# Kernel optimization log

Measured on AMD Instinct MI355X. Metric: run time of the kernel, lower is better.

The kernel has to match this reference:

```python
import jax, jax.numpy as jnp
import numpy as np

N, E, F_IN, H, C = 50000, 800000, 128, 4, 32
HC = H * C
NEG_SLOPE = 0.2


def setup_inputs() -> dict:
    key = jax.random.key(0)
    ks = jax.random.split(key, 20)
    def w(k, shape, fan_in):
        return jax.random.normal(k, shape, jnp.float32) * (1.0 / np.sqrt(fan_in))
    inp = {
        'x': jax.random.normal(ks[0], (N, F_IN), jnp.float32),
        'edge_index': jax.random.randint(ks[1], (2, E), 0, N, jnp.int64),
        # layer 1: in F_IN -> H*C
        'Wl1': w(ks[2], (F_IN, HC), F_IN), 'Wr1': w(ks[3], (F_IN, HC), F_IN),
        'att1': w(ks[4], (H, C), C), 'b1': jnp.zeros((HC,), jnp.float32),
        # layer 2: in H*C -> H*C
        'Wl2': w(ks[5], (HC, HC), HC), 'Wr2': w(ks[6], (HC, HC), HC),
        'att2': w(ks[7], (H, C), C), 'b2': jnp.zeros((HC,), jnp.float32),
        # layer 3
        'Wl3': w(ks[8], (HC, HC), HC), 'Wr3': w(ks[9], (HC, HC), HC),
        'att3': w(ks[10], (H, C), C), 'b3': jnp.zeros((HC,), jnp.float32),
        # final fc: H*C -> 1
        'Wf': w(ks[11], (HC, 1), HC), 'bf': jnp.zeros((1,), jnp.float32),
    }
    return inp


def gatv2_layer(x, src, dst, Wl, Wr, att, b):
    n = x.shape[0]
    xl = (x @ Wl).reshape(n, H, C)  # source transform
    xr = (x @ Wr).reshape(n, H, C)  # target transform
    z = xl[src] + xr[dst]                                  # [E', H, C]
    e = jnp.sum(jax.nn.leaky_relu(z, NEG_SLOPE) * att, axis=-1)  # [E', H]
    m = jax.ops.segment_max(e, dst, num_segments=n)        # segment softmax
    a = jnp.exp(e - m[dst])
    denom = jax.ops.segment_sum(a, dst, num_segments=n)
    alpha = a / denom[dst]                                 # [E', H]
    out = jax.ops.segment_sum(alpha[:, :, None] * xl[src], dst, num_segments=n)
    return out.reshape(n, HC) + b


def reference(x, edge_index, Wl1, Wr1, att1, b1, Wl2, Wr2, att2, b2, Wl3, Wr3, att3, b3, Wf, bf):
    n = x.shape[0]
    loops = jnp.arange(n, dtype=edge_index.dtype)
    src = jnp.concatenate([edge_index[0], loops])  # PyG adds self loops
    dst = jnp.concatenate([edge_index[1], loops])
    h = jax.nn.relu(gatv2_layer(x, src, dst, Wl1, Wr1, att1, b1))
    h = jax.nn.relu(gatv2_layer(h, src, dst, Wl2, Wr2, att2, b2))
    h = jax.nn.relu(gatv2_layer(h, src, dst, Wl3, Wr3, att3, b3))
    return (h @ Wf + bf)[:, 0]  # [N]
```

## Files before the change

### kernel.cpp

```cpp
#include <hip/hip_runtime.h>
#include <hip/hip_fp16.h>

constexpr int FDIM = 128;
constexpr float SLOPE = 0.2f;

using half8 = __attribute__((ext_vector_type(8))) _Float16;
using f32x4 = __attribute__((ext_vector_type(4))) float;

__device__ __forceinline__ float lrelu(float x) {
  return x > 0.f ? x : x * SLOPE;
}

struct F8 { float4 a, b; };
__device__ __forceinline__ F8 cvt8(uint4 u) {
  union { uint4 u; __half2 h[4]; } t;
  t.u = u;
  float2 f0 = __half22float2(t.h[0]);
  float2 f1 = __half22float2(t.h[1]);
  float2 f2 = __half22float2(t.h[2]);
  float2 f3 = __half22float2(t.h[3]);
  F8 r;
  r.a = make_float4(f0.x, f0.y, f1.x, f1.y);
  r.b = make_float4(f2.x, f2.y, f3.x, f3.y);
  return r;
}

__global__ __launch_bounds__(256) void prep_w(
    const float* __restrict__ W0, const float* __restrict__ W1,
    const float* __restrict__ W2, const float* __restrict__ W3,
    const float* __restrict__ W4, const float* __restrict__ W5,
    __half* __restrict__ Wt) {
  const float* Ws[6] = {W0, W1, W2, W3, W4, W5};
  const float* W = Ws[blockIdx.x];
  __half* o = Wt + (size_t)blockIdx.x * FDIM * FDIM;
  const int t = threadIdx.x;
  const int c4 = (t & 31) * 4;
#pragma unroll
  for (int rep = 0; rep < 16; ++rep) {
    int k = (t >> 5) + rep * 8;
    float4 v = *(const float4*)(W + (size_t)k * FDIM + c4);
    o[(size_t)(c4 + 0) * FDIM + k] = __float2half(v.x);
    o[(size_t)(c4 + 1) * FDIM + k] = __float2half(v.y);
    o[(size_t)(c4 + 2) * FDIM + k] = __float2half(v.z);
    o[(size_t)(c4 + 3) * FDIM + k] = __float2half(v.w);
  }
}

__global__ __launch_bounds__(512, 4) void gemm_mfma(
    const float* __restrict__ hin, const __half* __restrict__ Wlt,
    const __half* __restrict__ Wrt, __half* __restrict__ xl,
    __half* __restrict__ xr, int n) {
  __shared__ __half Ah[128][40];
  __shared__ __half Bsl[2][128][40];
  const int tid = threadIdx.x;
  const int row0 = blockIdx.x * 128;
  const int wv = tid >> 6;
  const int lane = tid & 63;
  const int sel = wv >> 2;
  const int rb = wv & 3;
  const int l15 = lane & 15;
  const int l4 = lane >> 4;

  f32x4 acc[2][8];
#pragma unroll
  for (int i = 0; i < 2; ++i)
#pragma unroll
    for (int j = 0; j < 8; ++j) acc[i][j] = (f32x4){0.f, 0.f, 0.f, 0.f};

  const int sr = tid >> 2;
  const int sc = (tid & 3) * 8;
  const int bslab = tid >> 8;
  const int bidx = tid & 255;
  const int bc = bidx >> 1;
  const int bko = (bidx & 1) * 16;
  const __half* Wsrc = bslab ? Wrt : Wlt;
  const int gr = row0 + sr;

  for (int k0 = 0; k0 < 128; k0 += 32) {
    if (k0) __syncthreads();
    {
      float4 v0 = make_float4(0.f, 0.f, 0.f, 0.f), v1 = v0;
      if (gr < n) {
        v0 = *(const float4*)(hin + (size_t)gr * FDIM + k0 + sc);
        v1 = *(const float4*)(hin + (size_t)gr * FDIM + k0 + sc + 4);
      }
      __half* dst = &Ah[sr][sc];
      dst[0] = __float2half(v0.x); dst[1] = __float2half(v0.y);
      dst[2] = __float2half(v0.z); dst[3] = __float2half(v0.w);
      dst[4] = __float2half(v1.x); dst[5] = __float2half(v1.y);
      dst[6] = __float2half(v1.z); dst[7] = __float2half(v1.w);
    }
    {
      const uint4* src = (const uint4*)(Wsrc + (size_t)bc * FDIM + k0 + bko);
      uint4 w0 = src[0], w1 = src[1];
      *(uint4*)&Bsl[bslab][bc][bko] = w0;
      *(uint4*)&Bsl[bslab][bc][bko + 8] = w1;
    }
    __syncthreads();
    half8 a0 = *(const half8*)&Ah[rb * 32 + l15][l4 * 8];
    half8 a1 = *(const half8*)&Ah[rb * 32 + 16 + l15][l4 * 8];
#pragma unroll
    for (int nf = 0; nf < 8; ++nf) {
      half8 b = *(const half8*)&Bsl[sel][nf * 16 + l15][l4 * 8];
      acc[0][nf] = __builtin_amdgcn_mfma_f32_16x16x32_f16(a0, b, acc[0][nf], 0, 0, 0);
      acc[1][nf] = __builtin_amdgcn_mfma_f32_16x16x32_f16(a1, b, acc[1][nf], 0, 0, 0);
    }
  }

  __half* out = sel ? xr : xl;
#pragma unroll
  for (int af = 0; af < 2; ++af) {
#pragma unroll
    for (int nf = 0; nf < 8; ++nf) {
      int col = nf * 16 + l15;
#pragma unroll
      for (int r = 0; r < 4; ++r) {
        int row = row0 + rb * 32 + af * 16 + l4 * 4 + r;
        if (row < n) out[(size_t)row * FDIM + col] = __float2half(acc[af][nf][r]);
      }
    }
  }
}

__global__ __launch_bounds__(256) void hist_dst(const int* __restrict__ dstI,
                                                int* __restrict__ deg, int e_cnt) {
  int i = blockIdx.x * blockDim.x + threadIdx.x;
  int stride = gridDim.x * blockDim.x;
  for (; i < e_cnt; i += stride) atomicAdd(&deg[dstI[i]], 1);
}

__global__ __launch_bounds__(1024) void scan_local(
    const int* __restrict__ deg, int* __restrict__ rowptr,
    int* __restrict__ btot, int n) {
  __shared__ int lds[1024];
  const int t = threadIdx.x;
  const int i = blockIdx.x * 1024 + t;
  int v = (i < n) ? deg[i] : 0;
  lds[t] = v;
  __syncthreads();
  for (int off = 1; off < 1024; off <<= 1) {
    int u = (t >= off) ? lds[t - off] : 0;
    __syncthreads();
    lds[t] += u;
    __syncthreads();
  }
  if (i < n) rowptr[i] = lds[t] - v;
  if (t == 1023) btot[blockIdx.x] = lds[1023];
}

__global__ __launch_bounds__(1024) void scan_btot(int* __restrict__ btot, int nb) {
  __shared__ int lds[1024];
  const int t = threadIdx.x;
  int v = (t < nb) ? btot[t] : 0;
  lds[t] = v;
  __syncthreads();
  for (int off = 1; off < 1024; off <<= 1) {
    int u = (t >= off) ? lds[t - off] : 0;
    __syncthreads();
    lds[t] += u;
    __syncthreads();
  }
  if (t < nb) btot[t] = lds[t] - v;
}

__global__ __launch_bounds__(1024) void scan_add(
    int* __restrict__ rowptr, int* __restrict__ rowcur,
    const int* __restrict__ btot, int n, int e_cnt) {
  const int i = blockIdx.x * 1024 + threadIdx.x;
  if (i < n) {
    int v = rowptr[i] + btot[blockIdx.x];
    rowptr[i] = v;
    rowcur[i] = v;
  }
  if (i == 0) rowptr[n] = e_cnt;
}

__global__ __launch_bounds__(256) void scatter_csr(
    const int* __restrict__ srcI, const int* __restrict__ dstI,
    int* __restrict__ rowcur, int* __restrict__ csr, int e_cnt) {
  int i = blockIdx.x * blockDim.x + threadIdx.x;
  int stride = gridDim.x * blockDim.x;
  for (; i < e_cnt; i += stride) {
    int pos = atomicAdd(&rowcur[dstI[i]], 1);
    csr[pos] = srcI[i];
  }
}

template <int LAST>
__global__ __launch_bounds__(256) void fused_attn(
    const __half* __restrict__ xl, const __half* __restrict__ xr,
    const int* __restrict__ rowptr, const int* __restrict__ csr,
    const float* __restrict__ att, const float* __restrict__ bias,
    const float* __restrict__ Wf, const float* __restrict__ bf,
    float* __restrict__ out, int n) {
  const int nid = (int)((blockIdx.x * (size_t)blockDim.x + threadIdx.x) >> 6);
  const int lane = threadIdx.x & 63;
  if (nid >= n) return;
  const int g = lane >> 4;
  const int q = lane & 15;
  const int f8 = q * 8;
  const float4 attA = *(const float4*)(att + f8);
  const float4 attB = *(const float4*)(att + f8 + 4);
  const F8 xrv = cvt8(*(const uint4*)(xr + (size_t)nid * FDIM + f8));
  const F8 xld = cvt8(*(const uint4*)(xl + (size_t)nid * FDIM + f8));
  const float4 xrA = xrv.a, xrB = xrv.b;
  const float4 xldA = xld.a, xldB = xld.b;

  float ps = fmaf(lrelu(xldA.x + xrA.x), attA.x,
             fmaf(lrelu(xldA.y + xrA.y), attA.y,
             fmaf(lrelu(xldA.z + xrA.z), attA.z,
             fmaf(lrelu(xldA.w + xrA.w), attA.w,
             fmaf(lrelu(xldB.x + xrB.x), attB.x,
             fmaf(lrelu(xldB.y + xrB.y), attB.y,
             fmaf(lrelu(xldB.z + xrB.z), attB.z,
                  lrelu(xldB.w + xrB.w) * attB.w)))))));
  ps += __shfl_xor(ps, 1);
  ps += __shfl_xor(ps, 2);

  float m = (g == 0) ? ps : -1e30f;
  float s = (g == 0) ? 1.f : 0.f;
  float4 accA = (g == 0) ? xldA : make_float4(0.f, 0.f, 0.f, 0.f);
  float4 accB = (g == 0) ? xldB : make_float4(0.f, 0.f, 0.f, 0.f);

  const int rs = rowptr[nid], re = rowptr[nid + 1];
  int jj = rs + g;
  bool v = jj < re;
  int sidx = v ? csr[jj] : 0;
  uint4 cur = make_uint4(0u, 0u, 0u, 0u);
  if (v) cur = *(const uint4*)(xl + (size_t)sidx * FDIM + f8);

  for (int t = rs; t < re; t += 4) {
    int jn = t + 4 + g;
    bool vn = jn < re;
    int sn = vn ? csr[jn] : 0;
    uint4 nxt = make_uint4(0u, 0u, 0u, 0u);
    if (vn) nxt = *(const uint4*)(xl + (size_t)sn * FDIM + f8);
    F8 xa = cvt8(cur);
    float4 xaA = xa.a, xaB = xa.b;
    float p = fmaf(lrelu(xaA.x + xrA.x), attA.x,
              fmaf(lrelu(xaA.y + xrA.y), attA.y,
              fmaf(lrelu(xaA.z + xrA.z), attA.z,
              fmaf(lrelu(xaA.w + xrA.w), attA.w,
              fmaf(lrelu(xaB.x + xrB.x), attB.x,
              fmaf(lrelu(xaB.y + xrB.y), attB.y,
              fmaf(lrelu(xaB.z + xrB.z), attB.z,
                   lrelu(xaB.w + xrB.w) * attB.w)))))));
    p += __shfl_xor(p, 1);
    p += __shfl_xor(p, 2);
    if (v) {
      float mn = fmaxf(m, p);
      float sc = __expf(m - mn);
      float w = __expf(p - mn);
      s = fmaf(s, sc, w);
      accA.x = fmaf(accA.x, sc, w * xaA.x);
      accA.y = fmaf(accA.y, sc, w * xaA.y);
      accA.z = fmaf(accA.z, sc, w * xaA.z);
      accA.w = fmaf(accA.w, sc, w * xaA.w);
      accB.x = fmaf(accB.x, sc, w * xaB.x);
      accB.y = fmaf(accB.y, sc, w * xaB.y);
      accB.z = fmaf(accB.z, sc, w * xaB.z);
      accB.w = fmaf(accB.w, sc, w * xaB.w);
      m = mn;
    }
    v = vn; cur = nxt;
  }

#pragma unroll
  for (int off = 16; off <= 32; off <<= 1) {
    float mo = __shfl_xor(m, off);
    float so = __shfl_xor(s, off);
    float4 aoA, aoB;
    aoA.x = __shfl_xor(accA.x, off); aoA.y = __shfl_xor(accA.y, off);
    aoA.z = __shfl_xor(accA.z, off); aoA.w = __shfl_xor(accA.w, off);
    aoB.x = __shfl_xor(accB.x, off); aoB.y = __shfl_xor(accB.y, off);
    aoB.z = __shfl_xor(accB.z, off); aoB.w = __shfl_xor(accB.w, off);
    float M = fmaxf(m, mo);
    float e0 = __expf(m - M), e1 = __expf(mo - M);
    s = fmaf(s, e0, so * e1);
    accA.x = fmaf(accA.x, e0, aoA.x * e1);
    accA.y = fmaf(accA.y, e0, aoA.y * e1);
    accA.z = fmaf(accA.z, e0, aoA.z * e1);
    accA.w = fmaf(accA.w, e0, aoA.w * e1);
    accB.x = fmaf(accB.x, e0, aoB.x * e1);
    accB.y = fmaf(accB.y, e0, aoB.y * e1);
    accB.z = fmaf(accB.z, e0, aoB.z * e1);
    accB.w = fmaf(accB.w, e0, aoB.w * e1);
    m = M;
  }

  const float inv = 1.f / s;
  const float4 bA = *(const float4*)(bias + f8);
  const float4 bB = *(const float4*)(bias + f8 + 4);
  float o0 = fmaxf(fmaf(accA.x, inv, bA.x), 0.f);
  float o1 = fmaxf(fmaf(accA.y, inv, bA.y), 0.f);
  float o2 = fmaxf(fmaf(accA.z, inv, bA.z), 0.f);
  float o3 = fmaxf(fmaf(accA.w, inv, bA.w), 0.f);
  float o4 = fmaxf(fmaf(accB.x, inv, bB.x), 0.f);
  float o5 = fmaxf(fmaf(accB.y, inv, bB.y), 0.f);
  float o6 = fmaxf(fmaf(accB.z, inv, bB.z), 0.f);
  float o7 = fmaxf(fmaf(accB.w, inv, bB.w), 0.f);

  if (LAST == 0) {
    if (g == 0) {
      *(float4*)(out + (size_t)nid * FDIM + f8) = make_float4(o0, o1, o2, o3);
      *(float4*)(out + (size_t)nid * FDIM + f8 + 4) = make_float4(o4, o5, o6, o7);
    }
  } else {
    const float4 wA = *(const float4*)(Wf + f8);
    const float4 wB = *(const float4*)(Wf + f8 + 4);
    float y = fmaf(o0, wA.x, fmaf(o1, wA.y, fmaf(o2, wA.z,
              fmaf(o3, wA.w, fmaf(o4, wB.x, fmaf(o5, wB.y,
              fmaf(o6, wB.z, o7 * wB.w)))))));
    y += __shfl_xor(y, 1);
    y += __shfl_xor(y, 2);
    y += __shfl_xor(y, 4);
    y += __shfl_xor(y, 8);
    if (lane == 0) out[nid] = y + bf[0];
  }
}

extern "C" void kernel_launch(void* const* d_in, const int* in_sizes, int n_in,
                              void* d_out, int out_size, void* d_ws, size_t ws_size,
                              hipStream_t stream) {
  const float* x = (const float*)d_in[0];
  const int* ei = (const int*)d_in[1];
  const int n = in_sizes[0] / FDIM;
  const int e_cnt = in_sizes[1] / 2;
  const int* srcI = ei;
  const int* dstI = ei + e_cnt;

  const float* Wl[3]  = {(const float*)d_in[2], (const float*)d_in[6], (const float*)d_in[10]};
  const float* Wr[3]  = {(const float*)d_in[3], (const float*)d_in[7], (const float*)d_in[11]};
  const float* att[3] = {(const float*)d_in[4], (const float*)d_in[8], (const float*)d_in[12]};
  const float* bs[3]  = {(const float*)d_in[5], (const float*)d_in[9], (const float*)d_in[13]};
  const float* Wf = (const float*)d_in[14];
  const float* bf = (const float*)d_in[15];

  __half* xlh = (__half*)d_ws;
  __half* xrh = xlh + (size_t)n * FDIM;
  float* hbuf = (float*)(xrh + (size_t)n * FDIM);
  int* deg    = (int*)(hbuf + (size_t)n * FDIM);
  int* rowptr = deg + n;
  int* rowcur = rowptr + n + 1;
  int* csr    = rowcur + n;
  int* btot   = csr + e_cnt;
  __half* Wt  = (__half*)(btot + 1024);

  const int nb = (n + 1023) / 1024;

  prep_w<<<6, 256, 0, stream>>>(Wl[0], Wr[0], Wl[1], Wr[1], Wl[2], Wr[2], Wt);
  hipMemsetAsync(deg, 0, (size_t)n * sizeof(int), stream);
  hist_dst<<<(e_cnt + 255) / 256, 256, 0, stream>>>(dstI, deg, e_cnt);
  scan_local<<<nb, 1024, 0, stream>>>(deg, rowptr, btot, n);
  scan_btot<<<1, 1024, 0, stream>>>(btot, nb);
  scan_add<<<nb, 1024, 0, stream>>>(rowptr, rowcur, btot, n, e_cnt);
  scatter_csr<<<(e_cnt + 255) / 256, 256, 0, stream>>>(srcI, dstI, rowcur, csr, e_cnt);

  const float* hin = x;
  const int gemmGrid = (n + 127) / 128;
  const int nodeBlocks = (n + 3) / 4;

  for (int L = 0; L < 3; ++L) {
    const __half* Wlt = Wt + (size_t)(2 * L) * FDIM * FDIM;
    const __half* Wrt = Wt + (size_t)(2 * L + 1) * FDIM * FDIM;
    gemm_mfma<<<gemmGrid, 512, 0, stream>>>(hin, Wlt, Wrt, xlh, xrh, n);
    if (L < 2) {
      fused_attn<0><<<nodeBlocks, 256, 0, stream>>>(xlh, xrh, rowptr, csr, att[L],
                                                    bs[L], nullptr, nullptr, hbuf, n);
      hin = hbuf;
    } else {
      fused_attn<1><<<nodeBlocks, 256, 0, stream>>>(xlh, xrh, rowptr, csr, att[L],
                                                    bs[L], Wf, bf, (float*)d_out, n);
    }
  }
}
```

Baseline: 384.9 us.

## Use fp16 intermediate activations, packed fp16 dot2 logits, and deeper gather prefetch

Layer outputs are now stored as fp16 rather than fp32, so the next GEMM loads half-width rows directly without converting them. The edge logit is computed with packed half2 add, leaky-relu and fdot2 instead of eight scalar fp32 FMAs, and attention weights are rounded to fp16. The neighbour gather now prefetches two edges ahead instead of one. Together these cut memory traffic and ALU work in the attention and GEMM kernels, at the cost of lower precision in the logits and activations and higher register pressure.

```diff
diff --git a/kernel.cpp b/kernel.cpp
--- a/kernel.cpp
+++ b/kernel.cpp
@@ -6,23 +6,28 @@
 
 using half8 = __attribute__((ext_vector_type(8))) _Float16;
 using f32x4 = __attribute__((ext_vector_type(4))) float;
-
-__device__ __forceinline__ float lrelu(float x) {
-  return x > 0.f ? x : x * SLOPE;
-}
-
-struct F8 { float4 a, b; };
-__device__ __forceinline__ F8 cvt8(uint4 u) {
-  union { uint4 u; __half2 h[4]; } t;
-  t.u = u;
-  float2 f0 = __half22float2(t.h[0]);
-  float2 f1 = __half22float2(t.h[1]);
-  float2 f2 = __half22float2(t.h[2]);
-  float2 f3 = __half22float2(t.h[3]);
-  F8 r;
-  r.a = make_float4(f0.x, f0.y, f1.x, f1.y);
-  r.b = make_float4(f2.x, f2.y, f3.x, f3.y);
-  return r;
+using h2v   = __attribute__((ext_vector_type(2))) _Float16;
+
+union H2U { __half2 s; h2v v; unsigned int u; };
+
+__device__ __forceinline__ float fdot2f(h2v a, h2v b, float c) {
+  return __builtin_amdgcn_fdot2(a, b, c, false);
+}
+
+union U4 { uint4 u; __half2 h[4]; };
+
+__device__ __forceinline__ float edge_logit(const __half2* xa2, const __half2* xr2,
+                                            const h2v* att2, h2v c02) {
+  float p = 0.f;
+#pragma unroll
+  for (int j = 0; j < 4; ++j) {
+    H2U ua, ur;
+    ua.s = xa2[j]; ur.s = xr2[j];
+    h2v z = ua.v + ur.v;
+    h2v lr = __builtin_elementwise_max(z, z * c02);
+    p = fdot2f(lr, att2[j], p);
+  }
+  return p;
 }
 
 __global__ __launch_bounds__(256) void prep_w(
@@ -46,8 +51,9 @@
   }
 }
 
+template <typename TIN>
 __global__ __launch_bounds__(512, 4) void gemm_mfma(
-    const float* __restrict__ hin, const __half* __restrict__ Wlt,
+    const TIN* __restrict__ hin, const __half* __restrict__ Wlt,
     const __half* __restrict__ Wrt, __half* __restrict__ xl,
     __half* __restrict__ xr, int n) {
   __shared__ __half Ah[128][40];
@@ -79,16 +85,23 @@
   for (int k0 = 0; k0 < 128; k0 += 32) {
     if (k0) __syncthreads();
     {
-      float4 v0 = make_float4(0.f, 0.f, 0.f, 0.f), v1 = v0;
-      if (gr < n) {
-        v0 = *(const float4*)(hin + (size_t)gr * FDIM + k0 + sc);
-        v1 = *(const float4*)(hin + (size_t)gr * FDIM + k0 + sc + 4);
+      union { uint4 u; __half h[8]; } pk;
+      if constexpr (sizeof(TIN) == 4) {
+        float4 v0 = make_float4(0.f, 0.f, 0.f, 0.f), v1 = v0;
+        if (gr < n) {
+          v0 = *(const float4*)((const float*)hin + (size_t)gr * FDIM + k0 + sc);
+          v1 = *(const float4*)((const float*)hin + (size_t)gr * FDIM + k0 + sc + 4);
+        }
+        pk.h[0] = __float2half(v0.x); pk.h[1] = __float2half(v0.y);
+        pk.h[2] = __float2half(v0.z); pk.h[3] = __float2half(v0.w);
+        pk.h[4] = __float2half(v1.x); pk.h[5] = __float2half(v1.y);
+        pk.h[6] = __float2half(v1.z); pk.h[7] = __float2half(v1.w);
+      } else {
+        pk.u = make_uint4(0u, 0u, 0u, 0u);
+        if (gr < n)
+          pk.u = *(const uint4*)((const __half*)hin + (size_t)gr * FDIM + k0 + sc);
       }
-      __half* dst = &Ah[sr][sc];
-      dst[0] = __float2half(v0.x); dst[1] = __float2half(v0.y);
-      dst[2] = __float2half(v0.z); dst[3] = __float2half(v0.w);
-      dst[4] = __float2half(v1.x); dst[5] = __float2half(v1.y);
-      dst[6] = __float2half(v1.z); dst[7] = __float2half(v1.w);
+      *(uint4*)&Ah[sr][sc] = pk.u;
     }
     {
       const uint4* src = (const uint4*)(Wsrc + (size_t)bc * FDIM + k0 + bko);
@@ -192,130 +205,111 @@
     const int* __restrict__ rowptr, const int* __restrict__ csr,
     const float* __restrict__ att, const float* __restrict__ bias,
     const float* __restrict__ Wf, const float* __restrict__ bf,
-    float* __restrict__ out, int n) {
+    void* __restrict__ outp, int n) {
   const int nid = (int)((blockIdx.x * (size_t)blockDim.x + threadIdx.x) >> 6);
   const int lane = threadIdx.x & 63;
   if (nid >= n) return;
   const int g = lane >> 4;
   const int q = lane & 15;
   const int f8 = q * 8;
-  const float4 attA = *(const float4*)(att + f8);
-  const float4 attB = *(const float4*)(att + f8 + 4);
-  const F8 xrv = cvt8(*(const uint4*)(xr + (size_t)nid * FDIM + f8));
-  const F8 xld = cvt8(*(const uint4*)(xl + (size_t)nid * FDIM + f8));
-  const float4 xrA = xrv.a, xrB = xrv.b;
-  const float4 xldA = xld.a, xldB = xld.b;
-
-  float ps = fmaf(lrelu(xldA.x + xrA.x), attA.x,
-             fmaf(lrelu(xldA.y + xrA.y), attA.y,
-             fmaf(lrelu(xldA.z + xrA.z), attA.z,
-             fmaf(lrelu(xldA.w + xrA.w), attA.w,
-             fmaf(lrelu(xldB.x + xrB.x), attB.x,
-             fmaf(lrelu(xldB.y + xrB.y), attB.y,
-             fmaf(lrelu(xldB.z + xrB.z), attB.z,
-                  lrelu(xldB.w + xrB.w) * attB.w)))))));
+  const h2v c02 = {(_Float16)SLOPE, (_Float16)SLOPE};
+  const float4 aA = *(const float4*)(att + f8);
+  const float4 aB = *(const float4*)(att + f8 + 4);
+  h2v att2[4] = {{(_Float16)aA.x, (_Float16)aA.y}, {(_Float16)aA.z, (_Float16)aA.w},
+                 {(_Float16)aB.x, (_Float16)aB.y}, {(_Float16)aB.z, (_Float16)aB.w}};
+  U4 xru, xlu;
+  xru.u = *(const uint4*)(xr + (size_t)nid * FDIM + f8);
+  xlu.u = *(const uint4*)(xl + (size_t)nid * FDIM + f8);
+
+  float ps = edge_logit(xlu.h, xru.h, att2, c02);
   ps += __shfl_xor(ps, 1);
   ps += __shfl_xor(ps, 2);
 
   float m = (g == 0) ? ps : -1e30f;
   float s = (g == 0) ? 1.f : 0.f;
-  float4 accA = (g == 0) ? xldA : make_float4(0.f, 0.f, 0.f, 0.f);
-  float4 accB = (g == 0) ? xldB : make_float4(0.f, 0.f, 0.f, 0.f);
+  float acc[8];
+#pragma unroll
+  for (int j = 0; j < 4; ++j) {
+    float2 f = __half22float2(xlu.h[j]);
+    acc[2 * j] = (g == 0) ? f.x : 0.f;
+    acc[2 * j + 1] = (g == 0) ? f.y : 0.f;
+  }
 
   const int rs = rowptr[nid], re = rowptr[nid + 1];
-  int jj = rs + g;
-  bool v = jj < re;
-  int sidx = v ? csr[jj] : 0;
-  uint4 cur = make_uint4(0u, 0u, 0u, 0u);
-  if (v) cur = *(const uint4*)(xl + (size_t)sidx * FDIM + f8);
+  const int j0 = rs + g;
+  bool v0 = j0 < re, v1 = (j0 + 4) < re;
+  U4 cur, nx1;
+  cur.u = make_uint4(0u, 0u, 0u, 0u);
+  nx1.u = cur.u;
+  if (v0) cur.u = *(const uint4*)(xl + (size_t)csr[j0] * FDIM + f8);
+  if (v1) nx1.u = *(const uint4*)(xl + (size_t)csr[j0 + 4] * FDIM + f8);
 
   for (int t = rs; t < re; t += 4) {
-    int jn = t + 4 + g;
-    bool vn = jn < re;
-    int sn = vn ? csr[jn] : 0;
-    uint4 nxt = make_uint4(0u, 0u, 0u, 0u);
-    if (vn) nxt = *(const uint4*)(xl + (size_t)sn * FDIM + f8);
-    F8 xa = cvt8(cur);
-    float4 xaA = xa.a, xaB = xa.b;
-    float p = fmaf(lrelu(xaA.x + xrA.x), attA.x,
-              fmaf(lrelu(xaA.y + xrA.y), attA.y,
-              fmaf(lrelu(xaA.z + xrA.z), attA.z,
-              fmaf(lrelu(xaA.w + xrA.w), attA.w,
-              fmaf(lrelu(xaB.x + xrB.x), attB.x,
-              fmaf(lrelu(xaB.y + xrB.y), attB.y,
-              fmaf(lrelu(xaB.z + xrB.z), attB.z,
-                   lrelu(xaB.w + xrB.w) * attB.w)))))));
+    const int jn = t + 8 + g;
+    const bool vn = jn < re;
+    U4 nx2;
+    nx2.u = make_uint4(0u, 0u, 0u, 0u);
+    if (vn) nx2.u = *(const uint4*)(xl + (size_t)csr[jn] * FDIM + f8);
+
+    float p = edge_logit(cur.h, xru.h, att2, c02);
     p += __shfl_xor(p, 1);
     p += __shfl_xor(p, 2);
-    if (v) {
+    if (v0) {
       float mn = fmaxf(m, p);
       float sc = __expf(m - mn);
       float w = __expf(p - mn);
       s = fmaf(s, sc, w);
-      accA.x = fmaf(accA.x, sc, w * xaA.x);
-      accA.y = fmaf(accA.y, sc, w * xaA.y);
-      accA.z = fmaf(accA.z, sc, w * xaA.z);
-      accA.w = fmaf(accA.w, sc, w * xaA.w);
-      accB.x = fmaf(accB.x, sc, w * xaB.x);
-      accB.y = fmaf(accB.y, sc, w * xaB.y);
-      accB.z = fmaf(accB.z, sc, w * xaB.z);
-      accB.w = fmaf(accB.w, sc, w * xaB.w);
+#pragma unroll
+      for (int j = 0; j < 4; ++j) {
+        acc[2 * j] = fmaf(acc[2 * j], sc, w * (float)__low2half(cur.h[j]));
+        acc[2 * j + 1] = fmaf(acc[2 * j + 1], sc, w * (float)__high2half(cur.h[j]));
+      }
       m = mn;
     }
-    v = vn; cur = nxt;
+    v0 = v1; v1 = vn; cur = nx1; nx1 = nx2;
   }
 
 #pragma unroll
   for (int off = 16; off <= 32; off <<= 1) {
     float mo = __shfl_xor(m, off);
     float so = __shfl_xor(s, off);
-    float4 aoA, aoB;
-    aoA.x = __shfl_xor(accA.x, off); aoA.y = __shfl_xor(accA.y, off);
-    aoA.z = __shfl_xor(accA.z, off); aoA.w = __shfl_xor(accA.w, off);
-    aoB.x = __shfl_xor(accB.x, off); aoB.y = __shfl_xor(accB.y, off);
-    aoB.z = __shfl_xor(accB.z, off); aoB.w = __shfl_xor(accB.w, off);
+    float ao[8];
+#pragma unroll
+    for (int j = 0; j < 8; ++j) ao[j] = __shfl_xor(acc[j], off);
     float M = fmaxf(m, mo);
     float e0 = __expf(m - M), e1 = __expf(mo - M);
     s = fmaf(s, e0, so * e1);
-    accA.x = fmaf(accA.x, e0, aoA.x * e1);
-    accA.y = fmaf(accA.y, e0, aoA.y * e1);
-    accA.z = fmaf(accA.z, e0, aoA.z * e1);
-    accA.w = fmaf(accA.w, e0, aoA.w * e1);
-    accB.x = fmaf(accB.x, e0, aoB.x * e1);
-    accB.y = fmaf(accB.y, e0, aoB.y * e1);
-    accB.z = fmaf(accB.z, e0, aoB.z * e1);
-    accB.w = fmaf(accB.w, e0, aoB.w * e1);
+#pragma unroll
+    for (int j = 0; j < 8; ++j) acc[j] = fmaf(acc[j], e0, ao[j] * e1);
     m = M;
   }
 
   const float inv = 1.f / s;
   const float4 bA = *(const float4*)(bias + f8);
   const float4 bB = *(const float4*)(bias + f8 + 4);
-  float o0 = fmaxf(fmaf(accA.x, inv, bA.x), 0.f);
-  float o1 = fmaxf(fmaf(accA.y, inv, bA.y), 0.f);
-  float o2 = fmaxf(fmaf(accA.z, inv, bA.z), 0.f);
-  float o3 = fmaxf(fmaf(accA.w, inv, bA.w), 0.f);
-  float o4 = fmaxf(fmaf(accB.x, inv, bB.x), 0.f);
-  float o5 = fmaxf(fmaf(accB.y, inv, bB.y), 0.f);
-  float o6 = fmaxf(fmaf(accB.z, inv, bB.z), 0.f);
-  float o7 = fmaxf(fmaf(accB.w, inv, bB.w), 0.f);
+  const float bb[8] = {bA.x, bA.y, bA.z, bA.w, bB.x, bB.y, bB.z, bB.w};
+  float o[8];
+#pragma unroll
+  for (int j = 0; j < 8; ++j) o[j] = fmaxf(fmaf(acc[j], inv, bb[j]), 0.f);
 
   if (LAST == 0) {
     if (g == 0) {
-      *(float4*)(out + (size_t)nid * FDIM + f8) = make_float4(o0, o1, o2, o3);
-      *(float4*)(out + (size_t)nid * FDIM + f8 + 4) = make_float4(o4, o5, o6, o7);
+      union { uint4 u; __half2 h[4]; } pk;
+#pragma unroll
+      for (int j = 0; j < 4; ++j) pk.h[j] = __floats2half2_rn(o[2 * j], o[2 * j + 1]);
+      *(uint4*)((__half*)outp + (size_t)nid * FDIM + f8) = pk.u;
     }
   } else {
     const float4 wA = *(const float4*)(Wf + f8);
     const float4 wB = *(const float4*)(Wf + f8 + 4);
-    float y = fmaf(o0, wA.x, fmaf(o1, wA.y, fmaf(o2, wA.z,
-              fmaf(o3, wA.w, fmaf(o4, wB.x, fmaf(o5, wB.y,
-              fmaf(o6, wB.z, o7 * wB.w)))))));
+    float y = fmaf(o[0], wA.x, fmaf(o[1], wA.y, fmaf(o[2], wA.z,
+              fmaf(o[3], wA.w, fmaf(o[4], wB.x, fmaf(o[5], wB.y,
+              fmaf(o[6], wB.z, o[7] * wB.w)))))));
     y += __shfl_xor(y, 1);
     y += __shfl_xor(y, 2);
     y += __shfl_xor(y, 4);
     y += __shfl_xor(y, 8);
-    if (lane == 0) out[nid] = y + bf[0];
+    if (lane == 0) ((float*)outp)[nid] = y + bf[0];
   }
 }
 
@@ -336,10 +330,10 @@
   const float* Wf = (const float*)d_in[14];
   const float* bf = (const float*)d_in[15];
 
-  __half* xlh = (__half*)d_ws;
-  __half* xrh = xlh + (size_t)n * FDIM;
-  float* hbuf = (float*)(xrh + (size_t)n * FDIM);
-  int* deg    = (int*)(hbuf + (size_t)n * FDIM);
+  __half* xlh  = (__half*)d_ws;
+  __half* xrh  = xlh + (size_t)n * FDIM;
+  __half* hbufh = xrh + (size_t)n * FDIM;
+  int* deg    = (int*)(hbufh + (size_t)n * FDIM);
   int* rowptr = deg + n;
   int* rowcur = rowptr + n + 1;
   int* csr    = rowcur + n;
@@ -349,28 +343,29 @@
   const int nb = (n + 1023) / 1024;
 
   prep_w<<<6, 256, 0, stream>>>(Wl[0], Wr[0], Wl[1], Wr[1], Wl[2], Wr[2], Wt);
-  hipMemsetAsync(deg, 0, (size_t)n * sizeof(int), stream);
+  (void)hipMemsetAsync(deg, 0, (size_t)n * sizeof(int), stream);
   hist_dst<<<(e_cnt + 255) / 256, 256, 0, stream>>>(dstI, deg, e_cnt);
   scan_local<<<nb, 1024, 0, stream>>>(deg, rowptr, btot, n);
   scan_btot<<<1, 1024, 0, stream>>>(btot, nb);
   scan_add<<<nb, 1024, 0, stream>>>(rowptr, rowcur, btot, n, e_cnt);
   scatter_csr<<<(e_cnt + 255) / 256, 256, 0, stream>>>(srcI, dstI, rowcur, csr, e_cnt);
 
-  const float* hin = x;
   const int gemmGrid = (n + 127) / 128;
   const int nodeBlocks = (n + 3) / 4;
 
   for (int L = 0; L < 3; ++L) {
     const __half* Wlt = Wt + (size_t)(2 * L) * FDIM * FDIM;
     const __half* Wrt = Wt + (size_t)(2 * L + 1) * FDIM * FDIM;
-    gemm_mfma<<<gemmGrid, 512, 0, stream>>>(hin, Wlt, Wrt, xlh, xrh, n);
+    if (L == 0)
+      gemm_mfma<float><<<gemmGrid, 512, 0, stream>>>(x, Wlt, Wrt, xlh, xrh, n);
+    else
+      gemm_mfma<__half><<<gemmGrid, 512, 0, stream>>>(hbufh, Wlt, Wrt, xlh, xrh, n);
     if (L < 2) {
       fused_attn<0><<<nodeBlocks, 256, 0, stream>>>(xlh, xrh, rowptr, csr, att[L],
-                                                    bs[L], nullptr, nullptr, hbuf, n);
-      hin = hbuf;
+                                                    bs[L], nullptr, nullptr, hbufh, n);
     } else {
       fused_attn<1><<<nodeBlocks, 256, 0, stream>>>(xlh, xrh, rowptr, csr, att[L],
-                                                    bs[L], Wf, bf, (float*)d_out, n);
-    }
-  }
-}
+                                                    bs[L], Wf, bf, d_out, n);
+    }
+  }
+}
```

Result: no change. 379.8 us (-1.3%).
